# Performance work log

Measured on AMD Instinct MI355X. Metric: run time of the kernel, lower is better.

## Reference

```python
import jax, jax.numpy as jnp
import numpy as np

HIDDEN = 2048
NUM_HEADS = 16
HEAD_DIM = HIDDEN // NUM_HEADS


def setup_inputs() -> dict:
    key = jax.random.key(0)
    ks = jax.random.split(key, 10)
    B, S = 2, 2048
    scale = 1.0 / np.sqrt(HIDDEN)
    inp = {
        "x": jax.random.normal(ks[0], (B, S, HIDDEN), dtype=jnp.float32),
        "attention_mask": jnp.zeros((B, S), dtype=jnp.float32),
        "Wq": jax.random.normal(ks[1], (HIDDEN, HIDDEN), dtype=jnp.float32) * scale,
        "bq": jnp.zeros((HIDDEN,), dtype=jnp.float32),
        "Wk": jax.random.normal(ks[2], (HIDDEN, HIDDEN), dtype=jnp.float32) * scale,
        "bk": jnp.zeros((HIDDEN,), dtype=jnp.float32),
        "Wv": jax.random.normal(ks[3], (HIDDEN, HIDDEN), dtype=jnp.float32) * scale,
        "bv": jnp.zeros((HIDDEN,), dtype=jnp.float32),
        "Wo": jax.random.normal(ks[4], (HIDDEN, HIDDEN), dtype=jnp.float32) * scale,
        "bo": jnp.zeros((HIDDEN,), dtype=jnp.float32),
    }
    return inp


def _split_heads(t):
    # [B, S, H*D] -> [B, H, S, D]
    B, S, _ = t.shape
    return t.reshape(B, S, NUM_HEADS, HEAD_DIM).transpose(0, 2, 1, 3)


def reference(x, attention_mask, Wq, bq, Wk, bk, Wv, bv, Wo, bo):
    B, S, _ = x.shape
    # Linear layers: y = x @ W^T + b (torch nn.Linear convention)
    q = _split_heads(x @ Wq.T + bq)  # [B, H, S, D]
    k = _split_heads(x @ Wk.T + bk)
    v = _split_heads(x @ Wv.T + bv)
    scale = 1.0 / jnp.sqrt(jnp.asarray(HEAD_DIM, dtype=x.dtype))
    scores = jnp.einsum("bhqd,bhkd->bhqk", q, k) * scale  # [B, H, S, S]
    scores = scores + attention_mask[:, None, None, :]  # additive mask broadcast
    attn = jax.nn.softmax(scores, axis=-1)
    out = jnp.einsum("bhqk,bhkd->bhqd", attn, v)  # [B, H, S, D]
    out = out.transpose(0, 2, 1, 3).reshape(B, S, HIDDEN)
    return out @ Wo.T + bo
```

## Files before the change

### kernel.cpp

```cpp
#include <hip/hip_runtime.h>
#include <math.h>

constexpr int S_LEN = 2048;
constexpr int HID   = 2048;
constexpr int NH    = 16;
constexpr int HD    = 128;

typedef __attribute__((ext_vector_type(8))) short short8;
typedef __attribute__((ext_vector_type(4))) float floatx4;

static __device__ __forceinline__ ushort f2bf(float f) {
  union { float f; unsigned u; } v; v.f = f;
  unsigned r = (v.u + 0x7fffu + ((v.u >> 16) & 1u)) >> 16;
  return (ushort)r;
}
static __device__ __forceinline__ ushort f2bf_fast(float f) {
  union { float f; unsigned u; } v; v.f = f;
  return (ushort)((v.u + 0x8000u) >> 16);
}

static __device__ __forceinline__ void glds16(const ushort* g, ushort* l) {
  __builtin_amdgcn_global_load_lds(
      (const __attribute__((address_space(1))) void*)g,
      (__attribute__((address_space(3))) void*)l, 16, 0, 0);
}

static __device__ __forceinline__ void barrier_raw() {
  __builtin_amdgcn_s_barrier();
  asm volatile("" ::: "memory");
}

static __device__ __forceinline__ void cvt4(ushort* dst, const float* src, size_t i) {
  const float4 v = ((const float4*)src)[i];
  ushort4 u = {f2bf(v.x), f2bf(v.y), f2bf(v.z), f2bf(v.w)};
  ((ushort4*)dst)[i] = u;
}

__global__ __launch_bounds__(256)
void convert_all(const float* __restrict__ x,
                 const float* __restrict__ wq, const float* __restrict__ wk,
                 const float* __restrict__ wv, const float* __restrict__ wo,
                 ushort* __restrict__ xb, ushort* __restrict__ wqb,
                 ushort* __restrict__ wkb, ushort* __restrict__ wvb,
                 ushort* __restrict__ wob) {
  const size_t gid = blockIdx.x * 256 + threadIdx.x;
  const size_t T = gridDim.x * 256;
  const size_t NX = (size_t)4096 * HID / 4;
  const size_t NW = (size_t)HID * HID / 4;
  for (size_t i = gid; i < NX; i += T) cvt4(xb, x, i);
  for (size_t i = gid; i < NW; i += T) {
    cvt4(wqb, wq, i);
    cvt4(wkb, wk, i);
    cvt4(wvb, wv, i);
    cvt4(wob, wo, i);
  }
}

template <bool BF16OUT>
__device__ __forceinline__
void gemm8_core(const ushort* __restrict__ A, const ushort* __restrict__ W,
                const float* __restrict__ bias, void* __restrict__ Cv,
                int m0, int n0) {
  __shared__ __align__(16) ushort lds[73728];
  constexpr int NT = HID / 64;

  const int tid  = threadIdx.x;
  const int lane = tid & 63;
  const int w    = tid >> 6;
  const int wm   = w >> 1, wn = w & 1;
  const int n16  = lane & 15, q4 = lane >> 4;
  const int n7   = n16 & 7;

  const int srow  = lane >> 3;
  const int sslot = lane & 7;
  const int sl    = sslot ^ srow;

  const ushort* asrc[4];
  const ushort* bsrc[2];
  #pragma unroll
  for (int c = 0; c < 4; ++c)
    asrc[c] = A + (size_t)(m0 + c*64 + w*8 + srow) * HID + sl*8;
  #pragma unroll
  for (int c = 0; c < 2; ++c)
    bsrc[c] = W + (size_t)(n0 + c*64 + w*8 + srow) * HID + sl*8;

  const int wofs = w * 512;

  floatx4 acc[4][4];
  #pragma unroll
  for (int i = 0; i < 4; ++i)
    #pragma unroll
    for (int j = 0; j < 4; ++j) acc[i][j] = (floatx4)0.f;

  auto stage_tile = [&](int t, ushort* base) {
    #pragma unroll
    for (int c = 0; c < 4; ++c)
      glds16(asrc[c] + (size_t)t*64, base + c*4096 + wofs);
    #pragma unroll
    for (int c = 0; c < 2; ++c)
      glds16(bsrc[c] + (size_t)t*64, base + 16384 + c*4096 + wofs);
  };

  stage_tile(0, lds);
  stage_tile(1, lds + 24576);

  for (int t = 0; t < NT; ++t) {
    if (t == NT - 1) asm volatile("s_waitcnt vmcnt(0)" ::: "memory");
    else             asm volatile("s_waitcnt vmcnt(6)" ::: "memory");
    barrier_raw();

    if (t + 2 < NT) stage_tile(t + 2, lds + (size_t)((t + 2) % 3) * 24576);

    const ushort* cA = lds + (size_t)(t % 3) * 24576;
    const ushort* cB = cA + 16384;

    short8 af[2][4], bf[2][4];
    #pragma unroll
    for (int kc = 0; kc < 2; ++kc) {
      #pragma unroll
      for (int mt = 0; mt < 4; ++mt)
        af[kc][mt] = *(const short8*)(cA + (wm*64 + mt*16 + n16)*64
                                         + (((kc*4 + q4) ^ n7) * 8));
      #pragma unroll
      for (int nt = 0; nt < 4; ++nt)
        bf[kc][nt] = *(const short8*)(cB + (wn*64 + nt*16 + n16)*64
                                         + (((kc*4 + q4) ^ n7) * 8));
    }
    #pragma unroll
    for (int kc = 0; kc < 2; ++kc) {
      __builtin_amdgcn_s_setprio(1);
      #pragma unroll
      for (int mt = 0; mt < 4; ++mt)
        #pragma unroll
        for (int nt = 0; nt < 4; ++nt)
          acc[mt][nt] = __builtin_amdgcn_mfma_f32_16x16x32_bf16(
              af[kc][mt], bf[kc][nt], acc[mt][nt], 0, 0, 0);
      __builtin_amdgcn_s_setprio(0);
    }
  }

  float bv4[4];
  #pragma unroll
  for (int nt = 0; nt < 4; ++nt) bv4[nt] = bias[n0 + wn*64 + nt*16 + n16];
  #pragma unroll
  for (int mt = 0; mt < 4; ++mt)
    #pragma unroll
    for (int nt = 0; nt < 4; ++nt)
      #pragma unroll
      for (int r = 0; r < 4; ++r) {
        const int row = m0 + wm*64 + mt*16 + q4*4 + r;
        const int col = n0 + wn*64 + nt*16 + n16;
        if (BF16OUT)
          ((ushort*)Cv)[(size_t)row * HID + col] = f2bf(acc[mt][nt][r] + bv4[nt]);
        else
          ((float*)Cv)[(size_t)row * HID + col] = acc[mt][nt][r] + bv4[nt];
      }
}

static __device__ __forceinline__ void tile_coords(int& m0, int& n0) {
  const int id = blockIdx.y * gridDim.x + blockIdx.x;
  const int s  = ((id & 7) << 5) | (id >> 3);
  m0 = (s >> 4) * 256;
  n0 = (s & 15) * 128;
}

__global__ __launch_bounds__(512, 2)
void gemm_qkv(const ushort* __restrict__ xb,
              const ushort* __restrict__ wqb, const ushort* __restrict__ wkb,
              const ushort* __restrict__ wvb,
              const float* __restrict__ bq, const float* __restrict__ bk,
              const float* __restrict__ bv,
              ushort* __restrict__ qb, ushort* __restrict__ kb_, ushort* __restrict__ vb) {
  const ushort* W; const float* bias; ushort* C;
  if (blockIdx.z == 0)      { W = wqb; bias = bq; C = qb;  }
  else if (blockIdx.z == 1) { W = wkb; bias = bk; C = kb_; }
  else                      { W = wvb; bias = bv; C = vb;  }
  int m0, n0; tile_coords(m0, n0);
  gemm8_core<true>(xb, W, bias, C, m0, n0);
}

__global__ __launch_bounds__(512, 2)
void gemm_o(const ushort* __restrict__ ao, const ushort* __restrict__ wob,
            const float* __restrict__ bo, float* __restrict__ out) {
  int m0, n0; tile_coords(m0, n0);
  gemm8_core<false>(ao, wob, bo, out, m0, n0);
}

__global__ __launch_bounds__(256)
void transpose_v(const ushort* __restrict__ vb, ushort* __restrict__ vt) {
  __shared__ ushort T[64][72];
  const int t  = threadIdx.x;
  const int bh = blockIdx.z;
  const int b = bh >> 4, h = bh & 15;
  const int s0 = blockIdx.x * 64;
  const int d0 = blockIdx.y * 64;
  {
    const int r = t >> 2, c = (t & 3) * 16;
    const ushort* src = vb + (size_t)(b*S_LEN + s0 + r)*HID + h*HD + d0 + c;
    *(uint4*)&T[r][c]     = *(const uint4*)src;
    *(uint4*)&T[r][c + 8] = *(const uint4*)(src + 8);
  }
  __syncthreads();
  {
    const int dd = t >> 2, c = (t & 3) * 16;
    ushort tmp[16];
    #pragma unroll
    for (int j = 0; j < 16; ++j) tmp[j] = T[c + j][dd];
    ushort* dst = vt + (size_t)((b*NH + h)*HD + d0 + dd)*S_LEN + s0 + c;
    *(uint4*)dst       = *(uint4*)tmp;
    *(uint4*)(dst + 8) = *(uint4*)(tmp + 8);
  }
}

__global__ __launch_bounds__(256, 2)
void attn_mfma(const ushort* __restrict__ qb, const ushort* __restrict__ kbuf,
               const ushort* __restrict__ vtb, const float* __restrict__ mask,
               ushort* __restrict__ ao) {
  __shared__ __align__(16) ushort SM[25600];

  const int tid  = threadIdx.x;
  const int w    = tid >> 6;
  const int lane = tid & 63;
  const int n16  = lane & 15;
  const int q4   = lane >> 4;
  const int n7   = n16 & 7;
  const int b  = blockIdx.y >> 4;
  const int h  = blockIdx.y & 15;
  const int q0 = blockIdx.x * 128;
  const float scale = 0.08838834764831845f;

  ushort* Ks = SM;
  ushort* Vs = SM + 8192;
  ushort* Pw = SM + 16384 + w * 2304;

  short8 aq[2][4];
  #pragma unroll
  for (int mt = 0; mt < 2; ++mt) {
    const ushort* qrow = qb + (size_t)(b*S_LEN + q0 + w*32 + mt*16 + n16)*HID + h*HD;
    #pragma unroll
    for (int kc = 0; kc < 4; ++kc)
      aq[mt][kc] = *(const short8*)(qrow + kc*32 + q4*8);
  }

  const ushort* ksrc[4];
  const ushort* vsrc[4];
  #pragma unroll
  for (int i = 0; i < 4; ++i) {
    const int p = (w*4 + i)*64 + lane;
    { const int rho = p >> 4, pc = p & 15;
      const int cl = (pc & 8) | ((pc ^ rho) & 7);
      ksrc[i] = kbuf + (size_t)(b*S_LEN + rho)*HID + h*HD + cl*8; }
    { const int rho = p >> 3, pc = p & 7;
      const int cl = (pc ^ rho) & 7;
      vsrc[i] = vtb + ((size_t)(b*NH + h)*HD + rho)*S_LEN + cl*8; }
  }

  floatx4 oacc[2][8];
  float lp[2][4];
  #pragma unroll
  for (int mt = 0; mt < 2; ++mt) {
    #pragma unroll
    for (int dt = 0; dt < 8; ++dt) oacc[mt][dt] = (floatx4)0.f;
    #pragma unroll
    for (int r = 0; r < 4; ++r) lp[mt][r] = 0.f;
  }

  #pragma unroll
  for (int i = 0; i < 4; ++i) glds16(ksrc[i], Ks + (w*4 + i)*512);
  #pragma unroll
  for (int i = 0; i < 4; ++i) glds16(vsrc[i], Vs + (w*4 + i)*512);

  for (int kb0 = 0; kb0 < S_LEN; kb0 += 64) {
    const int knext = (kb0 + 64 < S_LEN) ? kb0 + 64 : kb0;

    asm volatile("s_waitcnt vmcnt(4)" ::: "memory");
    barrier_raw();

    float mk[4];
    #pragma unroll
    for (int nt = 0; nt < 4; ++nt)
      mk[nt] = mask[(size_t)b*S_LEN + kb0 + nt*16 + n16];

    floatx4 acc[2][4];
    #pragma unroll
    for (int mt = 0; mt < 2; ++mt)
      #pragma unroll
      for (int nt = 0; nt < 4; ++nt) acc[mt][nt] = (floatx4)0.f;
    __builtin_amdgcn_s_setprio(1);
    #pragma unroll
    for (int nt = 0; nt < 4; ++nt) {
      #pragma unroll
      for (int kc = 0; kc < 4; ++kc) {
        const int cl = kc*4 + q4;
        const int pc = (cl & 8) | ((cl ^ n7) & 7);
        const short8 bk = *(const short8*)&Ks[(nt*16 + n16)*128 + pc*8];
        acc[0][nt] = __builtin_amdgcn_mfma_f32_16x16x32_bf16(aq[0][kc], bk, acc[0][nt], 0, 0, 0);
        acc[1][nt] = __builtin_amdgcn_mfma_f32_16x16x32_bf16(aq[1][kc], bk, acc[1][nt], 0, 0, 0);
      }
    }
    __builtin_amdgcn_s_setprio(0);

    barrier_raw();
    #pragma unroll
    for (int i = 0; i < 4; ++i)
      glds16(ksrc[i] + (size_t)knext * HID, Ks + (w*4 + i)*512);

    #pragma unroll
    for (int mt = 0; mt < 2; ++mt)
      #pragma unroll
      for (int r = 0; r < 4; ++r) {
        float p[4];
        #pragma unroll
        for (int nt = 0; nt < 4; ++nt) p[nt] = __expf(acc[mt][nt][r] * scale + mk[nt]);
        lp[mt][r] += (p[0] + p[1]) + (p[2] + p[3]);
        #pragma unroll
        for (int nt = 0; nt < 4; ++nt)
          Pw[(mt*16 + q4*4 + r)*72 + nt*16 + n16] = f2bf_fast(p[nt]);
      }

    asm volatile("s_waitcnt vmcnt(4)" ::: "memory");
    barrier_raw();

    __builtin_amdgcn_s_setprio(1);
    #pragma unroll
    for (int kc2 = 0; kc2 < 2; ++kc2) {
      const short8 ap0 = *(const short8*)&Pw[(0*16 + n16)*72 + kc2*32 + q4*8];
      const short8 ap1 = *(const short8*)&Pw[(1*16 + n16)*72 + kc2*32 + q4*8];
      const int clb = kc2*4 + q4;
      const int pcb = (clb ^ n7) & 7;
      #pragma unroll
      for (int dt = 0; dt < 8; ++dt) {
        const short8 bvf = *(const short8*)&Vs[(dt*16 + n16)*64 + pcb*8];
        oacc[0][dt] = __builtin_amdgcn_mfma_f32_16x16x32_bf16(ap0, bvf, oacc[0][dt], 0, 0, 0);
        oacc[1][dt] = __builtin_amdgcn_mfma_f32_16x16x32_bf16(ap1, bvf, oacc[1][dt], 0, 0, 0);
      }
    }
    __builtin_amdgcn_s_setprio(0);

    barrier_raw();
    #pragma unroll
    for (int i = 0; i < 4; ++i)
      glds16(vsrc[i] + knext, Vs + (w*4 + i)*512);
  }

  #pragma unroll
  for (int mt = 0; mt < 2; ++mt)
    #pragma unroll
    for (int r = 0; r < 4; ++r) {
      float l = lp[mt][r];
      l += __shfl_xor(l, 1);
      l += __shfl_xor(l, 2);
      l += __shfl_xor(l, 4);
      l += __shfl_xor(l, 8);
      lp[mt][r] = 1.0f / l;
    }

  __syncthreads();
  ushort* dump = SM + w * 4352;
  #pragma unroll
  for (int mt = 0; mt < 2; ++mt)
    #pragma unroll
    for (int r = 0; r < 4; ++r) {
      const int row = mt*16 + q4*4 + r;
      #pragma unroll
      for (int dt = 0; dt < 8; ++dt)
        dump[row*136 + dt*16 + n16] = f2bf(oacc[mt][dt][r] * lp[mt][r]);
    }
  const int drow = lane >> 1, dhalf = lane & 1;
  const size_t gbase = (size_t)(b*S_LEN + q0 + w*32 + drow)*HID + h*HD + dhalf*64;
  #pragma unroll
  for (int j = 0; j < 8; ++j)
    *(uint4*)&ao[gbase + j*8] = *(const uint4*)&dump[drow*136 + dhalf*64 + j*8];
}

extern "C" void kernel_launch(void* const* d_in, const int* in_sizes, int n_in,
                              void* d_out, int out_size, void* d_ws, size_t ws_size,
                              hipStream_t stream) {
  (void)n_in; (void)out_size; (void)ws_size;
  const float* x    = (const float*)d_in[0];
  const float* mask = (const float*)d_in[1];
  const float* Wq   = (const float*)d_in[2];
  const float* bq   = (const float*)d_in[3];
  const float* Wk   = (const float*)d_in[4];
  const float* bk   = (const float*)d_in[5];
  const float* Wv   = (const float*)d_in[6];
  const float* bv   = (const float*)d_in[7];
  const float* Wo   = (const float*)d_in[8];
  const float* bo   = (const float*)d_in[9];
  float* out = (float*)d_out;

  const int B = in_sizes[0] / (S_LEN * HID);
  const int M = B * S_LEN;
  const size_t MH = (size_t)M * HID;
  const size_t WW = (size_t)HID * HID;

  ushort* xb   = (ushort*)d_ws;
  ushort* wqb  = xb   + MH;
  ushort* wkb  = wqb  + WW;
  ushort* wvb  = wkb  + WW;
  ushort* wob  = wvb  + WW;
  ushort* qb   = wob  + WW;
  ushort* kbuf = qb   + MH;
  ushort* vb   = kbuf + MH;
  ushort* vt   = vb   + MH;
  ushort* ao   = xb;

  convert_all<<<512, 256, 0, stream>>>(x, Wq, Wk, Wv, Wo, xb, wqb, wkb, wvb, wob);
  gemm_qkv<<<dim3(HID/128, M/256, 3), 512, 0, stream>>>(xb, wqb, wkb, wvb, bq, bk, bv, qb, kbuf, vb);
  transpose_v<<<dim3(S_LEN/64, HD/64, B*NH), 256, 0, stream>>>(vb, vt);
  attn_mfma<<<dim3(S_LEN/128, B*NH), 256, 0, stream>>>(qb, kbuf, vt, mask, ao);
  gemm_o<<<dim3(HID/128, M/256), 512, 0, stream>>>(ao, wob, bo, out);
}
```

Baseline: 414.0 us.

## Split GEMM K-step into two half-phases interleaving global-to-LDS loads with MFMA

Restructures the projection GEMM main loop so each 64-wide K tile is processed in two 32-wide halves. Each half issues part of the next-next tile's global-to-LDS loads, reads its fragments from LDS, synchronizes, and then runs its MFMAs. The wait-and-barrier moves to the end of the iteration. The aim is to spread memory issue across the compute phase and shrink live fragment registers, at the cost of extra barriers per iteration.

```diff
diff --git a/kernel.cpp b/kernel.cpp
--- a/kernel.cpp
+++ b/kernel.cpp
@@ -92,51 +92,82 @@
     #pragma unroll
     for (int j = 0; j < 4; ++j) acc[i][j] = (floatx4)0.f;
 
-  auto stage_tile = [&](int t, ushort* base) {
-    #pragma unroll
-    for (int c = 0; c < 4; ++c)
-      glds16(asrc[c] + (size_t)t*64, base + c*4096 + wofs);
-    #pragma unroll
-    for (int c = 0; c < 2; ++c)
-      glds16(bsrc[c] + (size_t)t*64, base + 16384 + c*4096 + wofs);
-  };
-
-  stage_tile(0, lds);
-  stage_tile(1, lds + 24576);
+  {
+    ushort* b0 = lds;
+    ushort* b1 = lds + 24576;
+    #pragma unroll
+    for (int c = 0; c < 4; ++c) glds16(asrc[c],      b0 + c*4096 + wofs);
+    #pragma unroll
+    for (int c = 0; c < 2; ++c) glds16(bsrc[c],      b0 + 16384 + c*4096 + wofs);
+    #pragma unroll
+    for (int c = 0; c < 4; ++c) glds16(asrc[c] + 64, b1 + c*4096 + wofs);
+    #pragma unroll
+    for (int c = 0; c < 2; ++c) glds16(bsrc[c] + 64, b1 + 16384 + c*4096 + wofs);
+  }
+  asm volatile("s_waitcnt vmcnt(6)" ::: "memory");
+  barrier_raw();
 
   for (int t = 0; t < NT; ++t) {
-    if (t == NT - 1) asm volatile("s_waitcnt vmcnt(0)" ::: "memory");
-    else             asm volatile("s_waitcnt vmcnt(6)" ::: "memory");
-    barrier_raw();
-
-    if (t + 2 < NT) stage_tile(t + 2, lds + (size_t)((t + 2) % 3) * 24576);
-
     const ushort* cA = lds + (size_t)(t % 3) * 24576;
     const ushort* cB = cA + 16384;
-
-    short8 af[2][4], bf[2][4];
-    #pragma unroll
-    for (int kc = 0; kc < 2; ++kc) {
+    ushort* sb = lds + (size_t)((t + 2) % 3) * 24576;
+    const bool st = (t + 2 < NT);
+
+    if (st) {
+      glds16(asrc[0] + (size_t)(t+2)*64, sb + 0*4096 + wofs);
+      glds16(asrc[1] + (size_t)(t+2)*64, sb + 1*4096 + wofs);
+      glds16(asrc[2] + (size_t)(t+2)*64, sb + 2*4096 + wofs);
+    }
+    {
+      short8 af[4], bf[4];
       #pragma unroll
       for (int mt = 0; mt < 4; ++mt)
-        af[kc][mt] = *(const short8*)(cA + (wm*64 + mt*16 + n16)*64
-                                         + (((kc*4 + q4) ^ n7) * 8));
+        af[mt] = *(const short8*)(cA + (wm*64 + mt*16 + n16)*64 + ((q4 ^ n7) * 8));
       #pragma unroll
       for (int nt = 0; nt < 4; ++nt)
-        bf[kc][nt] = *(const short8*)(cB + (wn*64 + nt*16 + n16)*64
-                                         + (((kc*4 + q4) ^ n7) * 8));
-    }
-    #pragma unroll
-    for (int kc = 0; kc < 2; ++kc) {
+        bf[nt] = *(const short8*)(cB + (wn*64 + nt*16 + n16)*64 + ((q4 ^ n7) * 8));
+      barrier_raw();
+      asm volatile("s_waitcnt lgkmcnt(0)" ::: "memory");
+      __builtin_amdgcn_sched_barrier(0);
       __builtin_amdgcn_s_setprio(1);
       #pragma unroll
       for (int mt = 0; mt < 4; ++mt)
         #pragma unroll
         for (int nt = 0; nt < 4; ++nt)
           acc[mt][nt] = __builtin_amdgcn_mfma_f32_16x16x32_bf16(
-              af[kc][mt], bf[kc][nt], acc[mt][nt], 0, 0, 0);
+              af[mt], bf[nt], acc[mt][nt], 0, 0, 0);
       __builtin_amdgcn_s_setprio(0);
     }
+
+    if (st) {
+      glds16(asrc[3] + (size_t)(t+2)*64, sb + 3*4096 + wofs);
+      glds16(bsrc[0] + (size_t)(t+2)*64, sb + 16384 + 0*4096 + wofs);
+      glds16(bsrc[1] + (size_t)(t+2)*64, sb + 16384 + 1*4096 + wofs);
+    }
+    {
+      short8 af[4], bf[4];
+      #pragma unroll
+      for (int mt = 0; mt < 4; ++mt)
+        af[mt] = *(const short8*)(cA + (wm*64 + mt*16 + n16)*64 + (((4 + q4) ^ n7) * 8));
+      #pragma unroll
+      for (int nt = 0; nt < 4; ++nt)
+        bf[nt] = *(const short8*)(cB + (wn*64 + nt*16 + n16)*64 + (((4 + q4) ^ n7) * 8));
+      barrier_raw();
+      asm volatile("s_waitcnt lgkmcnt(0)" ::: "memory");
+      __builtin_amdgcn_sched_barrier(0);
+      __builtin_amdgcn_s_setprio(1);
+      #pragma unroll
+      for (int mt = 0; mt < 4; ++mt)
+        #pragma unroll
+        for (int nt = 0; nt < 4; ++nt)
+          acc[mt][nt] = __builtin_amdgcn_mfma_f32_16x16x32_bf16(
+              af[mt], bf[nt], acc[mt][nt], 0, 0, 0);
+      __builtin_amdgcn_s_setprio(0);
+    }
+
+    if (t + 2 < NT)       asm volatile("s_waitcnt vmcnt(6)" ::: "memory");
+    else if (t + 2 == NT) asm volatile("s_waitcnt vmcnt(0)" ::: "memory");
+    if (t < NT - 1) barrier_raw();
   }
 
   float bv4[4];
```

After: 384.7 us. 7.1% less time.

## Enlarge GEMM block tile to 256x256 with double-buffered LDS pipeline

Applied to the files above, without the earlier changes.

The shared GEMM core now computes a 256x256 output tile per block instead of 256x128. Waves are arranged 2x4, and each wave holds 8x4 MFMA accumulators, which raises arithmetic intensity per LDS load. The LDS staging moves from a triple buffer with one barrier per k-step to a double buffer with extra barriers around each prefetch, and tile swizzling and grid sizes are adjusted to match. Together with more blocks for the conversion kernel, this aims to cut global and LDS traffic per FLOP. The costs are higher register pressure, fewer blocks in the grid (256 for QKV, 64 for the output GEMM), and less overlap between loads and compute.

```diff
diff --git a/kernel.cpp b/kernel.cpp
--- a/kernel.cpp
+++ b/kernel.cpp
@@ -61,34 +61,32 @@
 void gemm8_core(const ushort* __restrict__ A, const ushort* __restrict__ W,
                 const float* __restrict__ bias, void* __restrict__ Cv,
                 int m0, int n0) {
-  __shared__ __align__(16) ushort lds[73728];
+  __shared__ __align__(16) ushort lds[65536];
   constexpr int NT = HID / 64;
 
   const int tid  = threadIdx.x;
   const int lane = tid & 63;
   const int w    = tid >> 6;
-  const int wm   = w >> 1, wn = w & 1;
+  const int wm   = w >> 2;
+  const int wn   = w & 3;
   const int n16  = lane & 15, q4 = lane >> 4;
   const int n7   = n16 & 7;
 
-  const int srow  = lane >> 3;
-  const int sslot = lane & 7;
-  const int sl    = sslot ^ srow;
+  const int srow = tid >> 3;
+  const int sl   = (tid & 7) ^ (srow & 7);
 
   const ushort* asrc[4];
-  const ushort* bsrc[2];
-  #pragma unroll
-  for (int c = 0; c < 4; ++c)
-    asrc[c] = A + (size_t)(m0 + c*64 + w*8 + srow) * HID + sl*8;
-  #pragma unroll
-  for (int c = 0; c < 2; ++c)
-    bsrc[c] = W + (size_t)(n0 + c*64 + w*8 + srow) * HID + sl*8;
-
+  const ushort* bsrc[4];
+  #pragma unroll
+  for (int c = 0; c < 4; ++c) {
+    asrc[c] = A + (size_t)(m0 + c*64 + srow) * HID + sl*8;
+    bsrc[c] = W + (size_t)(n0 + c*64 + srow) * HID + sl*8;
+  }
   const int wofs = w * 512;
 
-  floatx4 acc[4][4];
-  #pragma unroll
-  for (int i = 0; i < 4; ++i)
+  floatx4 acc[8][4];
+  #pragma unroll
+  for (int i = 0; i < 8; ++i)
     #pragma unroll
     for (int j = 0; j < 4; ++j) acc[i][j] = (floatx4)0.f;
 
@@ -97,71 +95,83 @@
     for (int c = 0; c < 4; ++c)
       glds16(asrc[c] + (size_t)t*64, base + c*4096 + wofs);
     #pragma unroll
-    for (int c = 0; c < 2; ++c)
+    for (int c = 0; c < 4; ++c)
       glds16(bsrc[c] + (size_t)t*64, base + 16384 + c*4096 + wofs);
   };
 
   stage_tile(0, lds);
-  stage_tile(1, lds + 24576);
+  stage_tile(1, lds + 32768);
+  asm volatile("s_waitcnt vmcnt(8)" ::: "memory");
+  barrier_raw();
 
   for (int t = 0; t < NT; ++t) {
-    if (t == NT - 1) asm volatile("s_waitcnt vmcnt(0)" ::: "memory");
-    else             asm volatile("s_waitcnt vmcnt(6)" ::: "memory");
+    const ushort* aB = lds + (size_t)(t & 1) * 32768;
+    const ushort* bB = aB + 16384;
+
+    short8 bfr[2][4];
+    #pragma unroll
+    for (int kc = 0; kc < 2; ++kc)
+      #pragma unroll
+      for (int nt = 0; nt < 4; ++nt)
+        bfr[kc][nt] = *(const short8*)(bB + (wn*64 + nt*16 + n16)*64
+                                          + (((kc*4 + q4) ^ n7) * 8));
+    #pragma unroll
+    for (int mh = 0; mh < 2; ++mh) {
+      short8 afr[2][4];
+      #pragma unroll
+      for (int kc = 0; kc < 2; ++kc)
+        #pragma unroll
+        for (int mi = 0; mi < 4; ++mi)
+          afr[kc][mi] = *(const short8*)(aB + (wm*128 + mh*64 + mi*16 + n16)*64
+                                            + (((kc*4 + q4) ^ n7) * 8));
+      __builtin_amdgcn_s_setprio(1);
+      #pragma unroll
+      for (int kc = 0; kc < 2; ++kc)
+        #pragma unroll
+        for (int mi = 0; mi < 4; ++mi)
+          #pragma unroll
+          for (int nt = 0; nt < 4; ++nt)
+            acc[mh*4 + mi][nt] = __builtin_amdgcn_mfma_f32_16x16x32_bf16(
+                afr[kc][mi], bfr[kc][nt], acc[mh*4 + mi][nt], 0, 0, 0);
+      __builtin_amdgcn_s_setprio(0);
+    }
+
     barrier_raw();
-
-    if (t + 2 < NT) stage_tile(t + 2, lds + (size_t)((t + 2) % 3) * 24576);
-
-    const ushort* cA = lds + (size_t)(t % 3) * 24576;
-    const ushort* cB = cA + 16384;
-
-    short8 af[2][4], bf[2][4];
-    #pragma unroll
-    for (int kc = 0; kc < 2; ++kc) {
-      #pragma unroll
-      for (int mt = 0; mt < 4; ++mt)
-        af[kc][mt] = *(const short8*)(cA + (wm*64 + mt*16 + n16)*64
-                                         + (((kc*4 + q4) ^ n7) * 8));
+    if (t + 2 < NT) {
+      stage_tile(t + 2, lds + (size_t)(t & 1) * 32768);
+      asm volatile("s_waitcnt vmcnt(8)" ::: "memory");
+      barrier_raw();
+    } else if (t + 1 < NT) {
+      asm volatile("s_waitcnt vmcnt(0)" ::: "memory");
+      barrier_raw();
+    }
+  }
+
+  float bv4[4];
+  #pragma unroll
+  for (int nt = 0; nt < 4; ++nt) bv4[nt] = bias[n0 + wn*64 + nt*16 + n16];
+  #pragma unroll
+  for (int mh = 0; mh < 2; ++mh)
+    #pragma unroll
+    for (int mi = 0; mi < 4; ++mi)
       #pragma unroll
       for (int nt = 0; nt < 4; ++nt)
-        bf[kc][nt] = *(const short8*)(cB + (wn*64 + nt*16 + n16)*64
-                                         + (((kc*4 + q4) ^ n7) * 8));
-    }
-    #pragma unroll
-    for (int kc = 0; kc < 2; ++kc) {
-      __builtin_amdgcn_s_setprio(1);
-      #pragma unroll
-      for (int mt = 0; mt < 4; ++mt)
         #pragma unroll
-        for (int nt = 0; nt < 4; ++nt)
-          acc[mt][nt] = __builtin_amdgcn_mfma_f32_16x16x32_bf16(
-              af[kc][mt], bf[kc][nt], acc[mt][nt], 0, 0, 0);
-      __builtin_amdgcn_s_setprio(0);
-    }
-  }
-
-  float bv4[4];
-  #pragma unroll
-  for (int nt = 0; nt < 4; ++nt) bv4[nt] = bias[n0 + wn*64 + nt*16 + n16];
-  #pragma unroll
-  for (int mt = 0; mt < 4; ++mt)
-    #pragma unroll
-    for (int nt = 0; nt < 4; ++nt)
-      #pragma unroll
-      for (int r = 0; r < 4; ++r) {
-        const int row = m0 + wm*64 + mt*16 + q4*4 + r;
-        const int col = n0 + wn*64 + nt*16 + n16;
-        if (BF16OUT)
-          ((ushort*)Cv)[(size_t)row * HID + col] = f2bf(acc[mt][nt][r] + bv4[nt]);
-        else
-          ((float*)Cv)[(size_t)row * HID + col] = acc[mt][nt][r] + bv4[nt];
-      }
+        for (int r = 0; r < 4; ++r) {
+          const int row = m0 + wm*128 + mh*64 + mi*16 + q4*4 + r;
+          const int col = n0 + wn*64 + nt*16 + n16;
+          if (BF16OUT)
+            ((ushort*)Cv)[(size_t)row * HID + col] = f2bf(acc[mh*4+mi][nt][r] + bv4[nt]);
+          else
+            ((float*)Cv)[(size_t)row * HID + col] = acc[mh*4+mi][nt][r] + bv4[nt];
+        }
 }
 
 static __device__ __forceinline__ void tile_coords(int& m0, int& n0) {
   const int id = blockIdx.y * gridDim.x + blockIdx.x;
-  const int s  = ((id & 7) << 5) | (id >> 3);
-  m0 = (s >> 4) * 256;
-  n0 = (s & 15) * 128;
+  const int s  = ((id & 7) << 4) | (id >> 3);
+  m0 = (s >> 3) * 256;
+  n0 = (s & 7) * 256;
 }
 
 __global__ __launch_bounds__(512, 2)
@@ -405,9 +415,9 @@
   ushort* vt   = vb   + MH;
   ushort* ao   = xb;
 
-  convert_all<<<512, 256, 0, stream>>>(x, Wq, Wk, Wv, Wo, xb, wqb, wkb, wvb, wob);
-  gemm_qkv<<<dim3(HID/128, M/256, 3), 512, 0, stream>>>(xb, wqb, wkb, wvb, bq, bk, bv, qb, kbuf, vb);
+  convert_all<<<1024, 256, 0, stream>>>(x, Wq, Wk, Wv, Wo, xb, wqb, wkb, wvb, wob);
+  gemm_qkv<<<dim3(HID/256, M/256, 3), 512, 0, stream>>>(xb, wqb, wkb, wvb, bq, bk, bv, qb, kbuf, vb);
   transpose_v<<<dim3(S_LEN/64, HD/64, B*NH), 256, 0, stream>>>(vb, vt);
   attn_mfma<<<dim3(S_LEN/128, B*NH), 256, 0, stream>>>(qb, kbuf, vt, mask, ao);
-  gemm_o<<<dim3(HID/128, M/256), 512, 0, stream>>>(ao, wob, bo, out);
-}
+  gemm_o<<<dim3(HID/256, M/256), 512, 0, stream>>>(ao, wob, bo, out);
+}
```

Result: slower. 428.1 us (+3.4%).
